# Kernel tuning notes

Measured on AMD Instinct MI355X. Metric: run time of the kernel, lower is better.

The kernel has to match this reference:

```python
import jax, jax.numpy as jnp
import numpy as np

N = 100000        # nodes
E = 1600000       # edges (N * avg_degree 16)
D_IN = 128
D_OUT = 32
OBS_T = 60        # observation_time -> decay table size 60*OBS_T = 3600
T_MAX = 60 * OBS_T


def setup_inputs() -> dict:
    key = jax.random.key(0)
    ks = jax.random.split(key, 8)
    inp = {
        "input": jax.random.normal(ks[0], (N, D_IN), dtype=jnp.float32),
        "W": jax.random.normal(ks[1], (D_IN, D_OUT), dtype=jnp.float32) * (np.sqrt(2.0) / np.sqrt(D_IN)),
        # decay weights are abs(normal(0, 0.02)) in the original; rand*0.04 is same scale
        "decay_weight1": jnp.abs(jax.random.normal(ks[2], (T_MAX, 1), dtype=jnp.float32) * 0.02),
        "decay_weight2": jnp.abs(jax.random.normal(ks[3], (T_MAX, 1), dtype=jnp.float32) * 0.02),
        "edge_row": jax.random.randint(ks[4], (E,), 0, N, dtype=jnp.int32),
        "edge_col": jax.random.randint(ks[5], (E,), 0, N, dtype=jnp.int32),
        # zero-based interval index; equals (adj_value - 1) of the original code
        "edge_time": jax.random.randint(ks[6], (E,), 0, T_MAX, dtype=jnp.int32),
        "arrive_time": jax.random.randint(ks[7], (N,), 0, T_MAX, dtype=jnp.int32),
        "observation_time": OBS_T,
    }
    return inp


def reference(input, W, decay_weight1, decay_weight2,
              edge_row, edge_col, edge_time, arrive_time, observation_time):
    n_nodes = input.shape[0]
    # h = relu(input @ W)  [N, D_OUT]
    h = jax.nn.relu(jnp.matmul(input, W))
    # one-hot(interval) @ decay_weight1 == embedding lookup  -> per-edge decay scalar
    decay = decay_weight1[edge_time, 0]                        # [E]
    # SpecialSpmm: out[i] = sum_{edges (i,j)} decay_e * h[j]  (gather-scale-scatter)
    msgs = decay[:, None] * h[edge_col]                        # [E, D_OUT]
    h_prime = jax.ops.segment_sum(msgs, edge_row, num_segments=n_nodes)
    # outlayer window decay: one-hot(60*T - arrive - 1) @ decay_weight2 == lookup
    win_idx = 60 * observation_time - arrive_time - 1          # [N] in [0, 60*T)
    h_prime = decay_weight2[win_idx, 0][:, None] * h_prime
    return h_prime
```

## Files before the change

### kernel.cpp

```cpp
#include <hip/hip_runtime.h>

#define N_NODES 100000
#define N_EDGES 1600000
#define D_IN    128
#define D_OUT   32
#define RPB     8
#define NB      (N_NODES / RPB)
#define CROWS   2048
#define NCB     49
#define FPC     (CROWS / RPB)
#define NSH     8
#define CAP_A   4500
#define DEPTH   48
#define CAPF    200
#define GRID_A  2048
#define EPB_A   ((N_EDGES + GRID_A - 1) / GRID_A)

typedef __attribute__((ext_vector_type(8))) short bf16x8;
typedef __attribute__((ext_vector_type(4))) float f32x4;

__device__ inline short f2bf(float f) {
    union { float f; unsigned u; } v; v.f = f;
    unsigned r = (v.u + 0x7FFFu + ((v.u >> 16) & 1u)) >> 16;
    return (short)r;
}
__device__ inline float bf2f(unsigned short b) {
    return __uint_as_float((unsigned)b << 16);
}

__global__ __launch_bounds__(256) void wconv_kernel(
    const float* __restrict__ W, short* __restrict__ WbT)
{
    const int i = blockIdx.x * 256 + threadIdx.x;
    if (i >= D_IN * D_OUT) return;
    const int k = i >> 5, c = i & 31;
    WbT[c * D_IN + k] = f2bf(W[i]);
}

__global__ __launch_bounds__(256) void gemm_mfma_kernel(
    const float* __restrict__ in, const short* __restrict__ WbT,
    unsigned short* __restrict__ h16)
{
    const int wave = threadIdx.x >> 6;
    const int lane = threadIdx.x & 63;
    const int r0   = blockIdx.x * 64 + wave * 16;
    const int c16  = lane & 15;
    const int quad = lane >> 4;

    int ra = r0 + c16;
    if (ra >= N_NODES) ra = N_NODES - 1;
    const float* arow = in + (size_t)ra * D_IN;

    f32x4 acc0 = {0.f, 0.f, 0.f, 0.f};
    f32x4 acc1 = {0.f, 0.f, 0.f, 0.f};

#pragma unroll
    for (int q = 0; q < 4; ++q) {
        const float* ap = arow + q * 32 + quad * 8;
        f32x4 a0 = *(const f32x4*)(ap);
        f32x4 a1 = *(const f32x4*)(ap + 4);
        bf16x8 af;
        af[0] = f2bf(a0.x); af[1] = f2bf(a0.y); af[2] = f2bf(a0.z); af[3] = f2bf(a0.w);
        af[4] = f2bf(a1.x); af[5] = f2bf(a1.y); af[6] = f2bf(a1.z); af[7] = f2bf(a1.w);
        bf16x8 b0 = *(const bf16x8*)(WbT + (c16)      * D_IN + q * 32 + quad * 8);
        bf16x8 b1 = *(const bf16x8*)(WbT + (c16 + 16) * D_IN + q * 32 + quad * 8);
        acc0 = __builtin_amdgcn_mfma_f32_16x16x32_bf16(af, b0, acc0, 0, 0, 0);
        acc1 = __builtin_amdgcn_mfma_f32_16x16x32_bf16(af, b1, acc1, 0, 0, 0);
    }

#pragma unroll
    for (int i = 0; i < 4; ++i) {
        const int rr = r0 + quad * 4 + i;
        if (rr < N_NODES) {
            h16[(size_t)rr * D_OUT + c16]      = (unsigned short)f2bf(fmaxf(acc0[i], 0.f));
            h16[(size_t)rr * D_OUT + c16 + 16] = (unsigned short)f2bf(fmaxf(acc1[i], 0.f));
        }
    }
}

__global__ __launch_bounds__(256) void phaseA_kernel(
    const int* __restrict__ erow, const int* __restrict__ ecol,
    const int* __restrict__ etime,
    int* __restrict__ gcur,
    uint2* __restrict__ segA)
{
    __shared__ uint2 lbin[NCB][DEPTH];
    __shared__ int   lcnt[NCB];
    __shared__ int   gbase[NCB];

    const int tid   = threadIdx.x;
    const int blk   = blockIdx.x;
    const int shard = blk & (NSH - 1);
    const int wv    = tid >> 6;
    const int ln    = tid & 63;

    if (tid < NCB) lcnt[tid] = 0;
    __syncthreads();

    const int e_beg = blk * EPB_A;
    const int e_end = min(e_beg + EPB_A, N_EDGES);

    for (int e = e_beg + tid; e < e_end; e += 256) {
        const int row = erow[e];
        const int cb  = row >> 11;
        uint2 p;
        p.x = (unsigned)ecol[e] | ((unsigned)(row & (CROWS - 1)) << 17);
        p.y = (unsigned)etime[e];
        const int pos = atomicAdd(&lcnt[cb], 1);
        if (pos < DEPTH) lbin[cb][pos] = p;
    }
    __syncthreads();

    if (tid < NCB) {
        const int c = min(lcnt[tid], DEPTH);
        gbase[tid] = atomicAdd(&gcur[(tid * NSH + shard) * 16], c);
    }
    __syncthreads();

    for (int bin = wv; bin < NCB; bin += 4) {
        const int c  = min(lcnt[bin], DEPTH);
        const int gb = gbase[bin];
        uint2* seg = segA + (size_t)(bin * NSH + shard) * CAP_A;
        for (int k = ln; k < c; k += 64) {
            if (gb + k < CAP_A) seg[gb + k] = lbin[bin][k];
        }
    }
}

__global__ __launch_bounds__(256) void phaseB_kernel(
    const int* __restrict__ gcur, const uint2* __restrict__ segA,
    int* __restrict__ fcur,
    unsigned* __restrict__ spk2)
{
    __shared__ int hist[FPC];
    __shared__ int curs[FPC];

    const int tid    = threadIdx.x;
    const int seg_id = blockIdx.x >> 1;
    const int half   = blockIdx.x & 1;
    const int cb     = seg_id >> 3;
    const int shard  = seg_id & 7;
    const int ntot   = min(gcur[(cb * NSH + shard) * 16], CAP_A);
    const int nh     = (ntot + 1) >> 1;
    const int beg    = half * nh;
    const int end    = min(ntot, beg + nh);
    const uint2* seg = segA + (size_t)(cb * NSH + shard) * CAP_A;

    hist[tid] = 0;
    __syncthreads();

    for (int i = beg + tid; i < end; i += 256)
        atomicAdd(&hist[(seg[i].x >> 20) & 255], 1);
    __syncthreads();

    {
        const int h  = hist[tid];
        const int fb = cb * FPC + tid;
        curs[tid] = (h && fb < NB) ? atomicAdd(&fcur[fb], h) : 0;
    }
    __syncthreads();

    for (int i = beg + tid; i < end; i += 256) {
        const uint2 p   = seg[i];
        const unsigned crl = (p.x >> 17) & 2047u;
        const int      fl  = crl >> 3;
        const unsigned rec = (p.x & 0x1FFFFu) | ((crl & 7u) << 17) | (p.y << 20);
        const int pos = atomicAdd(&curs[fl], 1);
        if (pos < CAPF)
            spk2[(size_t)(cb * FPC + fl) * CAPF + pos] = rec;
    }
}

__global__ __launch_bounds__(256) void bucket_reduce_kernel(
    const unsigned short* __restrict__ h16, const int* __restrict__ fcur,
    const unsigned* __restrict__ spk2, const float* __restrict__ dw1,
    const float* __restrict__ dw2, const int* __restrict__ arrive,
    const int* __restrict__ obs, float* __restrict__ out)
{
    __shared__ unsigned pk[CAPF];
    __shared__ unsigned pks[CAPF];
    __shared__ int bin[RPB];
    __shared__ int start[RPB + 1];
    __shared__ int cur[RPB];

    const int tid = threadIdx.x;
    const int b   = blockIdx.x;
    const int n   = min(fcur[b], CAPF);
    const unsigned* seg = spk2 + (size_t)b * CAPF;

    if (tid < RPB) bin[tid] = 0;
    __syncthreads();

    for (int i = tid; i < n; i += 256) {
        const unsigned p = seg[i];
        pk[i] = p;
        atomicAdd(&bin[(p >> 17) & 7], 1);
    }
    __syncthreads();

    if (tid == 0) {
        int a = 0;
#pragma unroll
        for (int r = 0; r < RPB; ++r) { start[r] = a; cur[r] = a; a += bin[r]; }
        start[RPB] = a;
    }
    __syncthreads();

    for (int i = tid; i < n; i += 256) {
        const unsigned p = pk[i];
        pks[atomicAdd(&cur[(p >> 17) & 7], 1)] = p;
    }
    __syncthreads();

    const int c = tid & 31;
    const int g = tid >> 5;
    const int T = 60 * obs[0];

    const int beg = start[g];
    const int end = start[g + 1];

    float acc = 0.f;
    int j = beg;
    for (; j + 4 <= end; j += 4) {
        const unsigned p0 = pks[j];
        const unsigned p1 = pks[j + 1];
        const unsigned p2 = pks[j + 2];
        const unsigned p3 = pks[j + 3];
        const float v0 = bf2f(h16[(size_t)(p0 & 0x1FFFF) * D_OUT + c]);
        const float v1 = bf2f(h16[(size_t)(p1 & 0x1FFFF) * D_OUT + c]);
        const float v2 = bf2f(h16[(size_t)(p2 & 0x1FFFF) * D_OUT + c]);
        const float v3 = bf2f(h16[(size_t)(p3 & 0x1FFFF) * D_OUT + c]);
        const float w0 = dw1[p0 >> 20];
        const float w1 = dw1[p1 >> 20];
        const float w2 = dw1[p2 >> 20];
        const float w3 = dw1[p3 >> 20];
        acc = fmaf(w0, v0, acc);
        acc = fmaf(w1, v1, acc);
        acc = fmaf(w2, v2, acc);
        acc = fmaf(w3, v3, acc);
    }
    for (; j < end; ++j) {
        const unsigned p = pks[j];
        acc = fmaf(dw1[p >> 20],
                   bf2f(h16[(size_t)(p & 0x1FFFF) * D_OUT + c]), acc);
    }

    const int r = b * RPB + g;
    const float sdw = dw2[T - arrive[r] - 1];
    out[(size_t)r * D_OUT + c] = acc * sdw;
}

extern "C" void kernel_launch(void* const* d_in, const int* in_sizes, int n_in,
                              void* d_out, int out_size, void* d_ws, size_t ws_size,
                              hipStream_t stream)
{
    const float* input  = (const float*)d_in[0];
    const float* W      = (const float*)d_in[1];
    const float* dw1    = (const float*)d_in[2];
    const float* dw2    = (const float*)d_in[3];
    const int*   erow   = (const int*)d_in[4];
    const int*   ecol   = (const int*)d_in[5];
    const int*   etime  = (const int*)d_in[6];
    const int*   arrive = (const int*)d_in[7];
    const int*   obs    = (const int*)d_in[8];

    float* out = (float*)d_out;

    char* p = (char*)d_ws;
    unsigned short* h16 = (unsigned short*)p;
    p += (size_t)N_NODES * D_OUT * 2;
    p = (char*)(((size_t)p + 255) & ~(size_t)255);
    short* WbT = (short*)p;
    p += D_IN * D_OUT * 2;
    p = (char*)(((size_t)p + 255) & ~(size_t)255);
    int* gcur = (int*)p;
    p += (size_t)NCB * NSH * 16 * 4;
    int* fcur = (int*)p;
    p += (size_t)NB * 4;
    p = (char*)(((size_t)p + 255) & ~(size_t)255);
    uint2* segA = (uint2*)p;
    p += (size_t)NCB * NSH * CAP_A * 8;
    p = (char*)(((size_t)p + 255) & ~(size_t)255);
    unsigned* spk2 = (unsigned*)p;

    hipMemsetAsync(gcur, 0, (size_t)(NCB * NSH * 16 + NB) * 4, stream);

    wconv_kernel<<<(D_IN * D_OUT + 255) / 256, 256, 0, stream>>>(W, WbT);
    gemm_mfma_kernel<<<(N_NODES + 63) / 64, 256, 0, stream>>>(input, WbT, h16);
    phaseA_kernel<<<GRID_A, 256, 0, stream>>>(erow, ecol, etime, gcur, segA);
    phaseB_kernel<<<NCB * NSH * 2, 256, 0, stream>>>(gcur, segA, fcur, spk2);
    bucket_reduce_kernel<<<NB, 256, 0, stream>>>(
        h16, fcur, spk2, dw1, dw2, arrive, obs, out);
}
```

Baseline: 184.7 us.

## Fuse W conversion, GEMM and edge binning into one heterogeneous launch

Merges the W-to-bf16 conversion, the MFMA GEMM and the phase-A edge binning into a single kernel whose blocks branch by index, so the independent GEMM and binning work can overlap and two launches disappear. Each GEMM block now converts W into shared memory itself, adding redundant work per block. Phase A also sends edges that overflow the local shared bin straight to the global segment with an atomic, where they were previously dropped. The reduce loop is unrolled to 8 with two partial accumulators.

Result: no change. 184.3 us (-0.3%).

```diff
diff --git a/kernel.cpp b/kernel.cpp
--- a/kernel.cpp
+++ b/kernel.cpp
@@ -13,6 +13,7 @@
 #define CAP_A   4500
 #define DEPTH   48
 #define CAPF    200
+#define GEMM_BLKS ((N_NODES + 63) / 64)
 #define GRID_A  2048
 #define EPB_A   ((N_EDGES + GRID_A - 1) / GRID_A)
 
@@ -28,101 +29,101 @@
     return __uint_as_float((unsigned)b << 16);
 }
 
-__global__ __launch_bounds__(256) void wconv_kernel(
-    const float* __restrict__ W, short* __restrict__ WbT)
-{
-    const int i = blockIdx.x * 256 + threadIdx.x;
-    if (i >= D_IN * D_OUT) return;
-    const int k = i >> 5, c = i & 31;
-    WbT[c * D_IN + k] = f2bf(W[i]);
-}
-
-__global__ __launch_bounds__(256) void gemm_mfma_kernel(
-    const float* __restrict__ in, const short* __restrict__ WbT,
-    unsigned short* __restrict__ h16)
-{
-    const int wave = threadIdx.x >> 6;
-    const int lane = threadIdx.x & 63;
-    const int r0   = blockIdx.x * 64 + wave * 16;
-    const int c16  = lane & 15;
-    const int quad = lane >> 4;
-
-    int ra = r0 + c16;
-    if (ra >= N_NODES) ra = N_NODES - 1;
-    const float* arow = in + (size_t)ra * D_IN;
-
-    f32x4 acc0 = {0.f, 0.f, 0.f, 0.f};
-    f32x4 acc1 = {0.f, 0.f, 0.f, 0.f};
-
-#pragma unroll
-    for (int q = 0; q < 4; ++q) {
-        const float* ap = arow + q * 32 + quad * 8;
-        f32x4 a0 = *(const f32x4*)(ap);
-        f32x4 a1 = *(const f32x4*)(ap + 4);
-        bf16x8 af;
-        af[0] = f2bf(a0.x); af[1] = f2bf(a0.y); af[2] = f2bf(a0.z); af[3] = f2bf(a0.w);
-        af[4] = f2bf(a1.x); af[5] = f2bf(a1.y); af[6] = f2bf(a1.z); af[7] = f2bf(a1.w);
-        bf16x8 b0 = *(const bf16x8*)(WbT + (c16)      * D_IN + q * 32 + quad * 8);
-        bf16x8 b1 = *(const bf16x8*)(WbT + (c16 + 16) * D_IN + q * 32 + quad * 8);
-        acc0 = __builtin_amdgcn_mfma_f32_16x16x32_bf16(af, b0, acc0, 0, 0, 0);
-        acc1 = __builtin_amdgcn_mfma_f32_16x16x32_bf16(af, b1, acc1, 0, 0, 0);
-    }
-
-#pragma unroll
-    for (int i = 0; i < 4; ++i) {
-        const int rr = r0 + quad * 4 + i;
-        if (rr < N_NODES) {
-            h16[(size_t)rr * D_OUT + c16]      = (unsigned short)f2bf(fmaxf(acc0[i], 0.f));
-            h16[(size_t)rr * D_OUT + c16 + 16] = (unsigned short)f2bf(fmaxf(acc1[i], 0.f));
-        }
-    }
-}
-
-__global__ __launch_bounds__(256) void phaseA_kernel(
-    const int* __restrict__ erow, const int* __restrict__ ecol,
+union SMemGA {
+    struct { short wbt[D_IN * D_OUT]; } g;
+    struct { uint2 lbin[NCB][DEPTH]; int lcnt[NCB]; int gbase[NCB]; } a;
+};
+
+__global__ __launch_bounds__(256) void gemm_phaseA_kernel(
+    const float* __restrict__ input, const float* __restrict__ W,
+    const int* __restrict__ erow,    const int* __restrict__ ecol,
     const int* __restrict__ etime,
+    unsigned short* __restrict__ h16,
     int* __restrict__ gcur,
     uint2* __restrict__ segA)
 {
-    __shared__ uint2 lbin[NCB][DEPTH];
-    __shared__ int   lcnt[NCB];
-    __shared__ int   gbase[NCB];
-
-    const int tid   = threadIdx.x;
-    const int blk   = blockIdx.x;
-    const int shard = blk & (NSH - 1);
-    const int wv    = tid >> 6;
-    const int ln    = tid & 63;
-
-    if (tid < NCB) lcnt[tid] = 0;
-    __syncthreads();
-
-    const int e_beg = blk * EPB_A;
-    const int e_end = min(e_beg + EPB_A, N_EDGES);
-
-    for (int e = e_beg + tid; e < e_end; e += 256) {
-        const int row = erow[e];
-        const int cb  = row >> 11;
-        uint2 p;
-        p.x = (unsigned)ecol[e] | ((unsigned)(row & (CROWS - 1)) << 17);
-        p.y = (unsigned)etime[e];
-        const int pos = atomicAdd(&lcnt[cb], 1);
-        if (pos < DEPTH) lbin[cb][pos] = p;
-    }
-    __syncthreads();
-
-    if (tid < NCB) {
-        const int c = min(lcnt[tid], DEPTH);
-        gbase[tid] = atomicAdd(&gcur[(tid * NSH + shard) * 16], c);
-    }
-    __syncthreads();
-
-    for (int bin = wv; bin < NCB; bin += 4) {
-        const int c  = min(lcnt[bin], DEPTH);
-        const int gb = gbase[bin];
-        uint2* seg = segA + (size_t)(bin * NSH + shard) * CAP_A;
-        for (int k = ln; k < c; k += 64) {
-            if (gb + k < CAP_A) seg[gb + k] = lbin[bin][k];
+    __shared__ SMemGA sm;
+    const int tid = threadIdx.x;
+
+    if (blockIdx.x < GEMM_BLKS) {
+        for (int i = tid; i < D_IN * D_OUT; i += 256) {
+            const int k = i >> 5, c = i & 31;
+            sm.g.wbt[c * D_IN + k] = f2bf(W[i]);
+        }
+        __syncthreads();
+
+        const int wave = tid >> 6;
+        const int lane = tid & 63;
+        const int r0   = blockIdx.x * 64 + wave * 16;
+        const int c16  = lane & 15;
+        const int quad = lane >> 4;
+
+        int ra = r0 + c16;
+        if (ra >= N_NODES) ra = N_NODES - 1;
+        const float* arow = input + (size_t)ra * D_IN;
+
+        f32x4 acc0 = {0.f, 0.f, 0.f, 0.f};
+        f32x4 acc1 = {0.f, 0.f, 0.f, 0.f};
+#pragma unroll
+        for (int q = 0; q < 4; ++q) {
+            const float* ap = arow + q * 32 + quad * 8;
+            f32x4 a0 = *(const f32x4*)(ap);
+            f32x4 a1 = *(const f32x4*)(ap + 4);
+            bf16x8 af;
+            af[0] = f2bf(a0.x); af[1] = f2bf(a0.y); af[2] = f2bf(a0.z); af[3] = f2bf(a0.w);
+            af[4] = f2bf(a1.x); af[5] = f2bf(a1.y); af[6] = f2bf(a1.z); af[7] = f2bf(a1.w);
+            bf16x8 b0 = *(const bf16x8*)(sm.g.wbt + (c16)      * D_IN + q * 32 + quad * 8);
+            bf16x8 b1 = *(const bf16x8*)(sm.g.wbt + (c16 + 16) * D_IN + q * 32 + quad * 8);
+            acc0 = __builtin_amdgcn_mfma_f32_16x16x32_bf16(af, b0, acc0, 0, 0, 0);
+            acc1 = __builtin_amdgcn_mfma_f32_16x16x32_bf16(af, b1, acc1, 0, 0, 0);
+        }
+#pragma unroll
+        for (int i = 0; i < 4; ++i) {
+            const int rr = r0 + quad * 4 + i;
+            if (rr < N_NODES) {
+                h16[(size_t)rr * D_OUT + c16]      = (unsigned short)f2bf(fmaxf(acc0[i], 0.f));
+                h16[(size_t)rr * D_OUT + c16 + 16] = (unsigned short)f2bf(fmaxf(acc1[i], 0.f));
+            }
+        }
+    } else {
+        const int blk   = blockIdx.x - GEMM_BLKS;
+        const int shard = blk & (NSH - 1);
+        const int wv    = tid >> 6;
+        const int ln    = tid & 63;
+
+        if (tid < NCB) sm.a.lcnt[tid] = 0;
+        __syncthreads();
+
+        const int e_beg = blk * EPB_A;
+        const int e_end = min(e_beg + EPB_A, N_EDGES);
+
+        for (int e = e_beg + tid; e < e_end; e += 256) {
+            const int row = erow[e];
+            const int cb  = row >> 11;
+            uint2 p;
+            p.x = (unsigned)ecol[e] | ((unsigned)(row & (CROWS - 1)) << 17);
+            p.y = (unsigned)etime[e];
+            const int pos = atomicAdd(&sm.a.lcnt[cb], 1);
+            if (pos < DEPTH) sm.a.lbin[cb][pos] = p;
+            else {
+                const int gp = atomicAdd(&gcur[(cb * NSH + shard) * 16], 1);
+                if (gp < CAP_A) segA[(size_t)(cb * NSH + shard) * CAP_A + gp] = p;
+            }
+        }
+        __syncthreads();
+
+        if (tid < NCB) {
+            const int c = min(sm.a.lcnt[tid], DEPTH);
+            sm.a.gbase[tid] = atomicAdd(&gcur[(tid * NSH + shard) * 16], c);
+        }
+        __syncthreads();
+
+        for (int bin = wv; bin < NCB; bin += 4) {
+            const int c  = min(sm.a.lcnt[bin], DEPTH);
+            const int gb = sm.a.gbase[bin];
+            uint2* seg = segA + (size_t)(bin * NSH + shard) * CAP_A;
+            for (int k = ln; k < c; k += 64)
+                if (gb + k < CAP_A) seg[gb + k] = sm.a.lbin[bin][k];
         }
     }
 }
@@ -221,23 +222,18 @@
 
     float acc = 0.f;
     int j = beg;
-    for (; j + 4 <= end; j += 4) {
-        const unsigned p0 = pks[j];
-        const unsigned p1 = pks[j + 1];
-        const unsigned p2 = pks[j + 2];
-        const unsigned p3 = pks[j + 3];
-        const float v0 = bf2f(h16[(size_t)(p0 & 0x1FFFF) * D_OUT + c]);
-        const float v1 = bf2f(h16[(size_t)(p1 & 0x1FFFF) * D_OUT + c]);
-        const float v2 = bf2f(h16[(size_t)(p2 & 0x1FFFF) * D_OUT + c]);
-        const float v3 = bf2f(h16[(size_t)(p3 & 0x1FFFF) * D_OUT + c]);
-        const float w0 = dw1[p0 >> 20];
-        const float w1 = dw1[p1 >> 20];
-        const float w2 = dw1[p2 >> 20];
-        const float w3 = dw1[p3 >> 20];
-        acc = fmaf(w0, v0, acc);
-        acc = fmaf(w1, v1, acc);
-        acc = fmaf(w2, v2, acc);
-        acc = fmaf(w3, v3, acc);
+    for (; j + 8 <= end; j += 8) {
+        float a0 = 0.f, a1 = 0.f;
+#pragma unroll
+        for (int u = 0; u < 8; u += 2) {
+            const unsigned pa = pks[j + u];
+            const unsigned pb = pks[j + u + 1];
+            const float va = bf2f(h16[(size_t)(pa & 0x1FFFF) * D_OUT + c]);
+            const float vb = bf2f(h16[(size_t)(pb & 0x1FFFF) * D_OUT + c]);
+            a0 = fmaf(dw1[pa >> 20], va, a0);
+            a1 = fmaf(dw1[pb >> 20], vb, a1);
+        }
+        acc += a0 + a1;
     }
     for (; j < end; ++j) {
         const unsigned p = pks[j];
@@ -269,9 +265,6 @@
     char* p = (char*)d_ws;
     unsigned short* h16 = (unsigned short*)p;
     p += (size_t)N_NODES * D_OUT * 2;
-    p = (char*)(((size_t)p + 255) & ~(size_t)255);
-    short* WbT = (short*)p;
-    p += D_IN * D_OUT * 2;
     p = (char*)(((size_t)p + 255) & ~(size_t)255);
     int* gcur = (int*)p;
     p += (size_t)NCB * NSH * 16 * 4;
@@ -285,9 +278,8 @@
 
     hipMemsetAsync(gcur, 0, (size_t)(NCB * NSH * 16 + NB) * 4, stream);
 
-    wconv_kernel<<<(D_IN * D_OUT + 255) / 256, 256, 0, stream>>>(W, WbT);
-    gemm_mfma_kernel<<<(N_NODES + 63) / 64, 256, 0, stream>>>(input, WbT, h16);
-    phaseA_kernel<<<GRID_A, 256, 0, stream>>>(erow, ecol, etime, gcur, segA);
+    gemm_phaseA_kernel<<<GEMM_BLKS + GRID_A, 256, 0, stream>>>(
+        input, W, erow, ecol, etime, h16, gcur, segA);
     phaseB_kernel<<<NCB * NSH * 2, 256, 0, stream>>>(gcur, segA, fcur, spk2);
     bucket_reduce_kernel<<<NB, 256, 0, stream>>>(
         h16, fcur, spk2, dw1, dw2, arrive, obs, out);
```
